# Kernel optimization log

Measured on AMD Instinct MI355X. Metric: run time of the kernel, lower is better.

## Reference

```python
import jax, jax.numpy as jnp
import numpy as np
import math

B, N, E = 1024, 128, 1024
IN_DIM, H, EDGE_DIM, L, OUT_DIM = 16, 128, 4, 4, 1


def setup_inputs() -> dict:
    key = jax.random.key(0)
    ks = jax.random.split(key, 32)
    def g(k, shape, scale):
        return jax.random.normal(k, shape, dtype=jnp.float32) * scale
    D_in = IN_DIM + 3
    s_in = 1.0 / math.sqrt(D_in)
    s_h = 1.0 / math.sqrt(H)
    inp = {
        'atom_types': jax.random.normal(ks[0], (B, N, IN_DIM), dtype=jnp.float32),
        'coords_spherical': jax.random.uniform(ks[1], (B, N, 3), dtype=jnp.float32),
        'edge_index': jax.random.randint(ks[2], (B, 2, E), 0, N, dtype=jnp.int32),
        'edge_attr': jax.random.uniform(ks[3], (B, E, EDGE_DIM), dtype=jnp.float32),
        # ComplexEmbedding: magnitude / phase linear maps
        'emb_Wm': g(ks[4], (D_in, H), s_in), 'emb_bm': jnp.zeros((H,), jnp.float32),
        'emb_Wp': g(ks[5], (D_in, H), s_in), 'emb_bp': jnp.zeros((H,), jnp.float32),
        # per-layer attention params (stacked over L layers)
        'Wq': g(ks[6], (L, H, H), s_h), 'bq': jnp.zeros((L, H), jnp.float32),
        'Wk': g(ks[7], (L, H, H), s_h), 'bk': jnp.zeros((L, H), jnp.float32),
        'Wvm': g(ks[8], (L, H, H), s_h), 'bvm': jnp.zeros((L, H), jnp.float32),
        'Wvp': g(ks[9], (L, H, H), s_h), 'bvp': jnp.zeros((L, H), jnp.float32),
        # EdgeBiasProjection: edge_attr -> scalar bias, plus learned distance penalty
        'We': g(ks[10], (L, EDGE_DIM, 1), 0.5), 'be': jnp.zeros((L, 1), jnp.float32),
        'dist_scale': jnp.full((L,), -0.5, jnp.float32),
        # LayerNorm over magnitude
        'ln_g': jnp.ones((L, H), jnp.float32), 'ln_b': jnp.zeros((L, H), jnp.float32),
        # RealProjection: concat(real, imag) -> hidden
        'rp_W': g(ks[11], (2 * H, H), 1.0 / math.sqrt(2 * H)), 'rp_b': jnp.zeros((H,), jnp.float32),
        # out_head: Linear(2H, H) -> SiLU -> Linear(H, out_dim)
        'h1_W': g(ks[12], (2 * H, H), 1.0 / math.sqrt(2 * H)), 'h1_b': jnp.zeros((H,), jnp.float32),
        'h2_W': g(ks[13], (H, OUT_DIM), s_h), 'h2_b': jnp.zeros((OUT_DIM,), jnp.float32),
    }
    return inp


def reference(atom_types, coords_spherical, edge_index, edge_attr,
              emb_Wm, emb_bm, emb_Wp, emb_bp,
              Wq, bq, Wk, bk, Wvm, bvm, Wvp, bvp,
              We, be, dist_scale, ln_g, ln_b,
              rp_W, rp_b, h1_W, h1_b, h2_W, h2_b):
    n_layers = Wq.shape[0]
    hidden = Wq.shape[-1]
    scale = 1.0 / math.sqrt(hidden)  # CAMBIO 1: sqrt(D) scaling

    def mol_fwd(feats, sph, ei, ea):
        n = feats.shape[0]
        x = jnp.concatenate([feats, sph], axis=-1)          # [N, in_dim+3]
        mag = x @ emb_Wm + emb_bm                            # [N, H]
        ph = x @ emb_Wp + emb_bp                             # [N, H]
        for l in range(n_layers):
            q = mag @ Wq[l] + bq[l]
            k = mag @ Wk[l] + bk[l]
            vm = mag @ Wvm[l] + bvm[l]
            vp = ph @ Wvp[l] + bvp[l]
            scores = (q @ k.T) * scale                       # [N, N]
            # CAMBIO 3/7: edge_attr -> scalar bias + learned distance penalty
            bvals = (ea @ We[l] + be[l])[:, 0] + dist_scale[l] * ea[:, 0]  # [E]
            bias = jnp.zeros((n, n), scores.dtype).at[ei[0], ei[1]].add(bvals)
            attn = jax.nn.softmax(scores + bias, axis=-1)
            new_mag = attn @ vm + mag                        # residual
            new_ph = attn @ vp + ph                          # residual
            # CAMBIO 6: LayerNorm over magnitude only
            mu = new_mag.mean(-1, keepdims=True)
            var = ((new_mag - mu) ** 2).mean(-1, keepdims=True)
            mag = ln_g[l] * (new_mag - mu) * jax.lax.rsqrt(var + 1e-5) + ln_b[l]
            ph = new_ph
        # CAMBIO 4: RealProjection concat(real, imag)
        real = mag * jnp.cos(ph)
        imag = mag * jnp.sin(ph)
        atom_repr = jnp.concatenate([real, imag], axis=-1) @ rp_W + rp_b  # [N, H]
        # CAMBIO 2: mean + sum pooling
        return jnp.concatenate([atom_repr.mean(0), atom_repr.sum(0)], axis=-1)  # [2H]

    pooled = jax.vmap(mol_fwd)(atom_types, coords_spherical, edge_index, edge_attr)  # [B, 2H]
    h = jax.nn.silu(pooled @ h1_W + h1_b)
    return h @ h2_W + h2_b                                   # [B, out_dim]
```

## Files before the change

### kernel.cpp

```cpp
#include <hip/hip_runtime.h>
#include <math.h>


typedef __attribute__((ext_vector_type(8)))  short s16x8;
typedef __attribute__((ext_vector_type(16))) float f32x16;

#define STR  136
#define LOFS 17408
#define MFMA(a, b, c) __builtin_amdgcn_mfma_f32_32x32x16_bf16(a, b, c, 0, 0, 0)
#define ROWP(reg) (((reg) & 3) + (((reg) >> 2) << 3) + (h5 << 2))

__device__ __forceinline__ unsigned short bfhi(float x) {
  unsigned u = __float_as_uint(x);
  return (unsigned short)((u + 0x7FFFu + ((u >> 16) & 1u)) >> 16);
}
__device__ __forceinline__ float bf2f(unsigned short h) {
  return __uint_as_float(((unsigned)h) << 16);
}

__device__ __forceinline__ void stageB64(short* SH, const f32x16& acc, int row,
                                         int colbase, int h5, float scl) {
  #pragma unroll
  for (int q = 0; q < 4; ++q) {
    int col = colbase + 8 * q + 4 * h5;
    float v0 = acc[4*q+0] * scl, v1 = acc[4*q+1] * scl;
    float v2 = acc[4*q+2] * scl, v3 = acc[4*q+3] * scl;
    unsigned short h0 = bfhi(v0), h1 = bfhi(v1), h2 = bfhi(v2), h3 = bfhi(v3);
    *(short4*)(SH + row * STR + col) = make_short4((short)h0,(short)h1,(short)h2,(short)h3);
    *(short4*)(SH + LOFS + row * STR + col) =
        make_short4((short)bfhi(v0 - bf2f(h0)), (short)bfhi(v1 - bf2f(h1)),
                    (short)bfhi(v2 - bf2f(h2)), (short)bfhi(v3 - bf2f(h3)));
  }
}

__device__ __forceinline__ void gemmTW2(f32x16* acc, const short* W, const short* BH,
                                        int mtile, int kbN, int ttb, int l31, int h5,
                                        int lane) {
  #pragma unroll 1
  for (int kb = 0; kb < kbN; ++kb) {
    const short* wp = W + (((mtile * 8 + kb) * 64 + lane) * 8);
    s16x8 ah = *(const s16x8*)wp;
    s16x8 al = *(const s16x8*)(wp + 32768);
    int k0 = kb * 16 + 8 * h5;
    #pragma unroll
    for (int j = 0; j < 2; ++j) {
      int brow = 32 * (ttb + j) + l31;
      s16x8 bh = *(const s16x8*)(BH + brow * STR + k0);
      s16x8 bl = *(const s16x8*)(BH + LOFS + brow * STR + k0);
      acc[j] = MFMA(ah, bh, acc[j]);
      acc[j] = MFMA(ah, bl, acc[j]);
      acc[j] = MFMA(al, bh, acc[j]);
    }
  }
}

__device__ __forceinline__ void gemmNW2(f32x16* acc, const short* AH, const short* W,
                                        int mblk, int ttb, int l31, int h5, int lane) {
  int arow = mblk + l31;
  #pragma unroll 1
  for (int kb = 0; kb < 8; ++kb) {
    int k0 = kb * 16 + 8 * h5;
    s16x8 ah = *(const s16x8*)(AH + arow * STR + k0);
    s16x8 al = *(const s16x8*)(AH + LOFS + arow * STR + k0);
    #pragma unroll
    for (int j = 0; j < 2; ++j) {
      const short* wp = W + ((((ttb + j) * 8 + kb) * 64 + lane) * 8);
      s16x8 bh = *(const s16x8*)wp;
      s16x8 bl = *(const s16x8*)(wp + 32768);
      acc[j] = MFMA(ah, bh, acc[j]);
      acc[j] = MFMA(ah, bl, acc[j]);
      acc[j] = MFMA(al, bh, acc[j]);
    }
  }
}

__device__ __forceinline__ void gemmLL2(f32x16* acc, const short* AH, const short* BH,
                                        int mblk, int ttb, int l31, int h5) {
  int arow = mblk + l31;
  #pragma unroll 1
  for (int kb = 0; kb < 8; ++kb) {
    int k0 = kb * 16 + 8 * h5;
    s16x8 ah = *(const s16x8*)(AH + arow * STR + k0);
    s16x8 al = *(const s16x8*)(AH + LOFS + arow * STR + k0);
    #pragma unroll
    for (int j = 0; j < 2; ++j) {
      int brow = 32 * (ttb + j) + l31;
      s16x8 bh = *(const s16x8*)(BH + brow * STR + k0);
      s16x8 bl = *(const s16x8*)(BH + LOFS + brow * STR + k0);
      acc[j] = MFMA(ah, bh, acc[j]);
      acc[j] = MFMA(ah, bl, acc[j]);
      acc[j] = MFMA(al, bh, acc[j]);
    }
  }
}

__global__ __launch_bounds__(256)
void prep0_kernel(const float* __restrict__ Wq, const float* __restrict__ Wk,
                  const float* __restrict__ bq,
                  float* __restrict__ wprime, float* __restrict__ u) {
  __shared__ float WkS[128 * 129];
  __shared__ float WqS[32 * 129];
  int l = blockIdx.x >> 2, ablk = blockIdx.x & 3;
  int t = threadIdx.x;
  const float* wk = Wk + (size_t)l * 16384;
  const float* wq = Wq + (size_t)l * 16384 + ablk * 32 * 128;
  for (int idx = t; idx < 16384; idx += 256)
    WkS[(idx >> 7) * 129 + (idx & 127)] = wk[idx];
  for (int idx = t; idx < 4096; idx += 256)
    WqS[(idx >> 7) * 129 + (idx & 127)] = wq[idx];
  __syncthreads();
  int a = t >> 3, bs = t & 7;
  float acc[16];
  #pragma unroll
  for (int j = 0; j < 16; ++j) acc[j] = 0.f;
  for (int c = 0; c < 128; ++c) {
    float qa = WqS[a * 129 + c];
    #pragma unroll
    for (int j = 0; j < 16; ++j) acc[j] += qa * WkS[(8 * j + bs) * 129 + c];
  }
  float* dst = wprime + ((size_t)l * 128 + ablk * 32 + a) * 128;
  #pragma unroll
  for (int j = 0; j < 16; ++j) dst[8 * j + bs] = acc[j];
  if (ablk == 0 && t < 128) {
    float s = 0.f;
    const float* bql = bq + l * 128;
    for (int c = 0; c < 128; ++c) s += WkS[t * 129 + c] * bql[c];
    u[l * 128 + t] = 0.08838834764831845f * s;
  }
}

__global__ __launch_bounds__(512)
void prep_kernel(const float* __restrict__ wprime,
                 const float* __restrict__ Wvm, const float* __restrict__ Wvp,
                 const float* __restrict__ rp_W,
                 const float* __restrict__ emb_Wm, const float* __restrict__ emb_Wp,
                 short* __restrict__ ws) {
  int mid = blockIdx.x >> 2, hblk = blockIdx.x & 3;
  int kb = threadIdx.x >> 6, lane = threadIdx.x & 63;
  const float* src;
  int krows = 128;
  if (mid < 4)        src = wprime + (size_t)mid * 16384;
  else if (mid < 8)   src = Wvm + (size_t)(mid - 4) * 16384;
  else if (mid < 12)  src = Wvp + (size_t)(mid - 8) * 16384;
  else if (mid == 12) src = rp_W;
  else if (mid == 13) src = rp_W + 16384;
  else if (mid == 14) { src = emb_Wm; krows = 19; }
  else                { src = emb_Wp; krows = 19; }
  int h = hblk * 32 + (lane & 31);
  int kbase = kb * 16 + ((lane >> 5) << 3);
  s16x8 H, L;
  #pragma unroll
  for (int j = 0; j < 8; ++j) {
    int k = kbase + j;
    float v = (k < krows) ? src[(size_t)k * 128 + h] : 0.f;
    unsigned short hi = bfhi(v);
    H[j] = (short)hi;
    L[j] = (short)bfhi(v - bf2f(hi));
  }
  short* dst = ws + (size_t)mid * 65536 + ((hblk * 8 + kb) * 64 + lane) * 8;
  *(s16x8*)dst = H;
  *(s16x8*)(dst + 32768) = L;
}

__global__ __launch_bounds__(512, 2)
void cpt_kernel(const float* __restrict__ atom_types,
                const float* __restrict__ coords,
                const int*   __restrict__ edge_index,
                const float* __restrict__ edge_attr,
                const float* __restrict__ emb_bm, const float* __restrict__ emb_bp,
                const float* __restrict__ bvm, const float* __restrict__ bvp,
                const float* __restrict__ We,  const float* __restrict__ be,
                const float* __restrict__ dist_scale,
                const float* __restrict__ ln_g, const float* __restrict__ ln_b,
                const float* __restrict__ rp_b,
                const float* __restrict__ h1_W, const float* __restrict__ h1_b,
                const float* __restrict__ h2_W, const float* __restrict__ h2_b,
                const short* __restrict__ wpre, const float* __restrict__ uArr,
                float* __restrict__ out)
{
  __shared__ __align__(16) short R1s[34816];
  __shared__ __align__(16) short R2s[34816];
  __shared__ float SCa[512];
  __shared__ float SCb[512];

  const int t = threadIdx.x, b = blockIdx.x;
  const int w = t >> 6, lane = t & 63, l31 = lane & 31, h5 = lane >> 5;
  const int wm = w >> 1, ttb = (w & 1) << 1;
  const int mblk = wm << 5;
  const float scale = 0.08838834764831845f;

  if (t < 128) {
    const float* xr = atom_types + ((size_t)b * 128 + t) * 16;
    const float* cr = coords + ((size_t)b * 128 + t) * 3;
    float xv[19];
    float4 a0 = *(const float4*)xr,       a1 = *(const float4*)(xr + 4);
    float4 a2 = *(const float4*)(xr + 8), a3 = *(const float4*)(xr + 12);
    xv[0]=a0.x; xv[1]=a0.y; xv[2]=a0.z; xv[3]=a0.w;
    xv[4]=a1.x; xv[5]=a1.y; xv[6]=a1.z; xv[7]=a1.w;
    xv[8]=a2.x; xv[9]=a2.y; xv[10]=a2.z; xv[11]=a2.w;
    xv[12]=a3.x; xv[13]=a3.y; xv[14]=a3.z; xv[15]=a3.w;
    xv[16]=cr[0]; xv[17]=cr[1]; xv[18]=cr[2];
    #pragma unroll
    for (int k = 0; k < 32; ++k) {
      float v = (k < 19) ? xv[k] : 0.f;
      unsigned short hh = bfhi(v);
      R1s[t * STR + k] = (short)hh;
      R1s[LOFS + t * STR + k] = (short)bfhi(v - bf2f(hh));
    }
  }
  __syncthreads();

  f32x16 magT[2], phT[2];
  {
    #pragma unroll
    for (int reg = 0; reg < 16; ++reg) {
      float bm = emb_bm[32 * wm + ROWP(reg)];
      float bp = emb_bp[32 * wm + ROWP(reg)];
      #pragma unroll
      for (int j = 0; j < 2; ++j) { magT[j][reg] = bm; phT[j][reg] = bp; }
    }
    gemmTW2(magT, wpre + (size_t)14 * 65536, R1s, wm, 2, ttb, l31, h5, lane);
    gemmTW2(phT,  wpre + (size_t)15 * 65536, R1s, wm, 2, ttb, l31, h5, lane);
  }

  for (int l = 0; l < 4; ++l) {
    const short* wpP  = wpre + (size_t)l * 65536;
    const short* wvmP = wpre + (size_t)(4 + l) * 65536;
    const short* wvpP = wpre + (size_t)(8 + l) * 65536;
    float* Bf = (float*)R2s;

    __syncthreads();
    #pragma unroll
    for (int j = 0; j < 2; ++j)
      stageB64(R1s, magT[j], 32 * (ttb + j) + l31, mblk, h5, 1.f);
    {
      float4 z4 = make_float4(0.f, 0.f, 0.f, 0.f);
      #pragma unroll
      for (int k = 0; k < 8; ++k) *(float4*)(Bf + (t + 512 * k) * 4) = z4;
    }
    {
      float ur[16];
      #pragma unroll
      for (int reg = 0; reg < 16; ++reg) ur[reg] = uArr[l * 128 + 32 * wm + ROWP(reg)];
      #pragma unroll
      for (int j = 0; j < 2; ++j) {
        float p = 0.f;
        #pragma unroll
        for (int reg = 0; reg < 16; ++reg) p += magT[j][reg] * ur[reg];
        p += __shfl_xor(p, 32);
        if (h5 == 0) SCa[wm * 128 + 32 * (ttb + j) + l31] = p;
      }
    }
    __syncthreads();

    {
      float w0 = We[l*4], w1 = We[l*4+1], w2 = We[l*4+2], w3 = We[l*4+3];
      float bel = be[l], dsl = dist_scale[l];
      #pragma unroll
      for (int k = 0; k < 2; ++k) {
        int e = t + 512 * k;
        int e0 = edge_index[(size_t)b * 2048 + e];
        int e1 = edge_index[(size_t)b * 2048 + 1024 + e];
        float4 ea = *(const float4*)(edge_attr + ((size_t)b * 1024 + e) * 4);
        float bv = ea.x*w0 + ea.y*w1 + ea.z*w2 + ea.w*w3 + bel + dsl*ea.x;
        atomicAdd(&Bf[e1 * 128 + e0], bv);
      }
    }

    f32x16 accT[2];
    #pragma unroll
    for (int j = 0; j < 2; ++j)
      #pragma unroll
      for (int reg = 0; reg < 16; ++reg) accT[j][reg] = 0.f;
    gemmTW2(accT, wpP, R1s, wm, 8, ttb, l31, h5, lane);
    __syncthreads();

    f32x16 accS[2];
    {
      float vj[16];
      #pragma unroll
      for (int reg = 0; reg < 16; ++reg) {
        int jj = 32 * wm + ROWP(reg);
        vj[reg] = SCa[jj] + SCa[128 + jj] + SCa[256 + jj] + SCa[384 + jj];
      }
      #pragma unroll
      for (int j = 0; j < 2; ++j) {
        #pragma unroll
        for (int reg = 0; reg < 16; ++reg)
          accS[j][reg] = Bf[(32 * wm + ROWP(reg)) * 128 + 32 * (ttb + j) + l31] + vj[reg];
      }
    }
    __syncthreads();
    #pragma unroll
    for (int j = 0; j < 2; ++j)
      stageB64(R2s, accT[j], 32 * (ttb + j) + l31, mblk, h5, scale);
    __syncthreads();

    gemmLL2(accS, R1s, R2s, mblk, ttb, l31, h5);

    #pragma unroll
    for (int j = 0; j < 2; ++j) {
      float m = accS[j][0];
      #pragma unroll
      for (int reg = 1; reg < 16; ++reg) m = fmaxf(m, accS[j][reg]);
      m = fmaxf(m, __shfl_xor(m, 32));
      if (h5 == 0) SCa[wm * 128 + 32 * (ttb + j) + l31] = m;
    }
    __syncthreads();
    #pragma unroll
    for (int j = 0; j < 2; ++j) {
      int i = 32 * (ttb + j) + l31;
      float mg = fmaxf(fmaxf(SCa[i], SCa[128 + i]), fmaxf(SCa[256 + i], SCa[384 + i]));
      float s = 0.f;
      #pragma unroll
      for (int reg = 0; reg < 16; ++reg) {
        float e = __expf(accS[j][reg] - mg);
        accS[j][reg] = e; s += e;
      }
      s += __shfl_xor(s, 32);
      if (h5 == 0) SCb[wm * 128 + i] = s;
    }
    __syncthreads();
    #pragma unroll
    for (int j = 0; j < 2; ++j) {
      int i = 32 * (ttb + j) + l31;
      float sg = SCb[i] + SCb[128 + i] + SCb[256 + i] + SCb[384 + i];
      float inv = 1.f / sg;
      #pragma unroll
      for (int reg = 0; reg < 16; ++reg) accS[j][reg] *= inv;
    }
    #pragma unroll
    for (int j = 0; j < 2; ++j)
      stageB64(R2s, accS[j], 32 * (ttb + j) + l31, mblk, h5, 1.f);

    {
      f32x16 accVM[2];
      #pragma unroll
      for (int j = 0; j < 2; ++j) {
        float bv = bvm[l * 128 + 32 * (ttb + j) + l31];
        #pragma unroll
        for (int reg = 0; reg < 16; ++reg) accVM[j][reg] = bv;
      }
      gemmNW2(accVM, R1s, wvmP, mblk, ttb, l31, h5, lane);
      __syncthreads();
      #pragma unroll
      for (int j = 0; j < 2; ++j)
        stageB64(R1s, accVM[j], 32 * (ttb + j) + l31, mblk, h5, 1.f);
      __syncthreads();
    }

    f32x16 accM[2];
    #pragma unroll
    for (int j = 0; j < 2; ++j) accM[j] = magT[j];
    gemmLL2(accM, R1s, R2s, mblk, ttb, l31, h5);

    {
      #pragma unroll
      for (int j = 0; j < 2; ++j) {
        float s = 0.f, q = 0.f;
        #pragma unroll
        for (int reg = 0; reg < 16; ++reg) { float v = accM[j][reg]; s += v; q += v*v; }
        s += __shfl_xor(s, 32); q += __shfl_xor(q, 32);
        if (h5 == 0) {
          SCa[wm * 128 + 32 * (ttb + j) + l31] = s;
          SCb[wm * 128 + 32 * (ttb + j) + l31] = q;
        }
      }
      __syncthreads();
      #pragma unroll
      for (int reg = 0; reg < 16; ++reg) {
        float gv = ln_g[l * 128 + 32 * wm + ROWP(reg)];
        float bv = ln_b[l * 128 + 32 * wm + ROWP(reg)];
        #pragma unroll
        for (int j = 0; j < 2; ++j) {
          int i = 32 * (ttb + j) + l31;
          float s = SCa[i] + SCa[128 + i] + SCa[256 + i] + SCa[384 + i];
          float q = SCb[i] + SCb[128 + i] + SCb[256 + i] + SCb[384 + i];
          float mu = s * (1.f / 128.f);
          float var = q * (1.f / 128.f) - mu * mu;
          float inv = 1.f / sqrtf(var + 1e-5f);
          magT[j][reg] = gv * ((accM[j][reg] - mu) * inv) + bv;
        }
      }
    }
    #pragma unroll
    for (int j = 0; j < 2; ++j)
      stageB64(R1s, phT[j], 32 * (ttb + j) + l31, mblk, h5, 1.f);
    __syncthreads();

    {
      f32x16 accV[2];
      #pragma unroll
      for (int j = 0; j < 2; ++j) {
        float bv = bvp[l * 128 + 32 * (ttb + j) + l31];
        #pragma unroll
        for (int reg = 0; reg < 16; ++reg) accV[j][reg] = bv;
      }
      gemmNW2(accV, R1s, wvpP, mblk, ttb, l31, h5, lane);
      __syncthreads();
      #pragma unroll
      for (int j = 0; j < 2; ++j)
        stageB64(R1s, accV[j], 32 * (ttb + j) + l31, mblk, h5, 1.f);
      __syncthreads();
    }

    f32x16 accP[2];
    #pragma unroll
    for (int j = 0; j < 2; ++j) accP[j] = phT[j];
    gemmLL2(accP, R1s, R2s, mblk, ttb, l31, h5);
    #pragma unroll
    for (int j = 0; j < 2; ++j) phT[j] = accP[j];
  }

  f32x16 reT[2], imT[2];
  #pragma unroll
  for (int j = 0; j < 2; ++j)
    #pragma unroll
    for (int reg = 0; reg < 16; ++reg) {
      float s_, c_;
      __sincosf(phT[j][reg], &s_, &c_);
      reT[j][reg] = magT[j][reg] * c_;
      imT[j][reg] = magT[j][reg] * s_;
    }
  __syncthreads();
  #pragma unroll
  for (int j = 0; j < 2; ++j) {
    stageB64(R1s, reT[j], 32 * (ttb + j) + l31, mblk, h5, 1.f);
    stageB64(R2s, imT[j], 32 * (ttb + j) + l31, mblk, h5, 1.f);
  }
  __syncthreads();
  f32x16 accR[2];
  #pragma unroll
  for (int reg = 0; reg < 16; ++reg) {
    float bv = rp_b[32 * wm + ROWP(reg)];
    #pragma unroll
    for (int j = 0; j < 2; ++j) accR[j][reg] = bv;
  }
  gemmTW2(accR, wpre + (size_t)12 * 65536, R1s, wm, 8, ttb, l31, h5, lane);
  gemmTW2(accR, wpre + (size_t)13 * 65536, R2s, wm, 8, ttb, l31, h5, lane);

  {
    float cs[16];
    #pragma unroll
    for (int reg = 0; reg < 16; ++reg) {
      float s = accR[0][reg] + accR[1][reg];
      s += __shfl_xor(s, 16); s += __shfl_xor(s, 8);
      s += __shfl_xor(s, 4);  s += __shfl_xor(s, 2); s += __shfl_xor(s, 1);
      cs[reg] = s;
    }
    if (l31 == 0) {
      #pragma unroll
      for (int reg = 0; reg < 16; ++reg)
        SCa[(w & 1) * 128 + 32 * wm + ROWP(reg)] = cs[reg];
    }
  }
  __syncthreads();
  if (t < 128) {
    float acc = h1_b[t];
    for (int i = 0; i < 128; ++i) {
      float c = SCa[i] + SCa[128 + i];
      acc += c * (h1_W[(size_t)i * 128 + t] * (1.f / 128.f) +
                  h1_W[(size_t)(128 + i) * 128 + t]);
    }
    float hv = acc / (1.f + __expf(-acc));
    SCb[t] = hv * h2_W[t];
  }
  __syncthreads();
  if (t < 64) {
    float s2 = SCb[t] + SCb[64 + t];
    #pragma unroll
    for (int off = 32; off >= 1; off >>= 1) s2 += __shfl_xor(s2, off);
    if (t == 0) out[b] = s2 + h2_b[0];
  }
}

extern "C" void kernel_launch(void* const* d_in, const int* in_sizes, int n_in,
                              void* d_out, int out_size, void* d_ws, size_t ws_size,
                              hipStream_t stream) {
  const float* atom_types = (const float*)d_in[0];
  const float* coords     = (const float*)d_in[1];
  const int*   edge_index = (const int*)  d_in[2];
  const float* edge_attr  = (const float*)d_in[3];
  const float* emb_Wm = (const float*)d_in[4];
  const float* emb_bm = (const float*)d_in[5];
  const float* emb_Wp = (const float*)d_in[6];
  const float* emb_bp = (const float*)d_in[7];
  const float* Wq  = (const float*)d_in[8];
  const float* bq  = (const float*)d_in[9];
  const float* Wk  = (const float*)d_in[10];
  const float* bk  = (const float*)d_in[11];
  const float* Wvm = (const float*)d_in[12];
  const float* bvm = (const float*)d_in[13];
  const float* Wvp = (const float*)d_in[14];
  const float* bvp = (const float*)d_in[15];
  const float* We  = (const float*)d_in[16];
  const float* be  = (const float*)d_in[17];
  const float* dist_scale = (const float*)d_in[18];
  const float* ln_g = (const float*)d_in[19];
  const float* ln_b = (const float*)d_in[20];
  const float* rp_W = (const float*)d_in[21];
  const float* rp_b = (const float*)d_in[22];
  const float* h1_W = (const float*)d_in[23];
  const float* h1_b = (const float*)d_in[24];
  const float* h2_W = (const float*)d_in[25];
  const float* h2_b = (const float*)d_in[26];
  float* out = (float*)d_out;
  (void)bk;
  short* wpre   = (short*)d_ws;
  float* uArr   = (float*)((char*)d_ws + (size_t)16 * 131072);
  float* wprime = (float*)((char*)d_ws + (size_t)16 * 131072 + 2048);

  hipLaunchKernelGGL(prep0_kernel, dim3(16), dim3(256), 0, stream,
                     Wq, Wk, bq, wprime, uArr);
  hipLaunchKernelGGL(prep_kernel, dim3(64), dim3(512), 0, stream,
                     wprime, Wvm, Wvp, rp_W, emb_Wm, emb_Wp, wpre);
  hipLaunchKernelGGL(cpt_kernel, dim3(1024), dim3(512), 0, stream,
                     atom_types, coords, edge_index, edge_attr,
                     emb_bm, emb_bp,
                     bvm, bvp,
                     We, be, dist_scale, ln_g, ln_b,
                     rp_b, h1_W, h1_b, h2_W, h2_b,
                     (const short*)wpre, (const float*)uArr, out);
}
```

Measured before the change: 621.8 us.

## Double block to 1024 threads with one 32x32 output tile per wave

The per-molecule kernel now launches 1024 threads (16 waves) instead of 512. Each wave owns a single 32-column tile rather than two, and all GEMM helpers, softmax, LayerNorm and the final reductions are rewritten for one accumulator per wave. Since shared memory limits each CU to about one block, the aim is twice as many resident waves to hide LDS and global latency, and fewer registers per thread. The cost is that each wave reloads its A/weight fragments on its own, so the per-MFMA load traffic is roughly doubled, and 1024-thread barriers get more expensive.

Measured after the change: 758.3 us. 22.0% more time.

```diff
diff --git a/kernel.cpp b/kernel.cpp
--- a/kernel.cpp
+++ b/kernel.cpp
@@ -33,64 +33,55 @@
   }
 }
 
-__device__ __forceinline__ void gemmTW2(f32x16* acc, const short* W, const short* BH,
-                                        int mtile, int kbN, int ttb, int l31, int h5,
+__device__ __forceinline__ void gemmTW1(f32x16& acc, const short* W, const short* BH,
+                                        int mtile, int kbN, int tt, int l31, int h5,
                                         int lane) {
+  int brow = 32 * tt + l31;
   #pragma unroll 1
   for (int kb = 0; kb < kbN; ++kb) {
     const short* wp = W + (((mtile * 8 + kb) * 64 + lane) * 8);
     s16x8 ah = *(const s16x8*)wp;
     s16x8 al = *(const s16x8*)(wp + 32768);
     int k0 = kb * 16 + 8 * h5;
-    #pragma unroll
-    for (int j = 0; j < 2; ++j) {
-      int brow = 32 * (ttb + j) + l31;
-      s16x8 bh = *(const s16x8*)(BH + brow * STR + k0);
-      s16x8 bl = *(const s16x8*)(BH + LOFS + brow * STR + k0);
-      acc[j] = MFMA(ah, bh, acc[j]);
-      acc[j] = MFMA(ah, bl, acc[j]);
-      acc[j] = MFMA(al, bh, acc[j]);
-    }
-  }
-}
-
-__device__ __forceinline__ void gemmNW2(f32x16* acc, const short* AH, const short* W,
-                                        int mblk, int ttb, int l31, int h5, int lane) {
+    s16x8 bh = *(const s16x8*)(BH + brow * STR + k0);
+    s16x8 bl = *(const s16x8*)(BH + LOFS + brow * STR + k0);
+    acc = MFMA(ah, bh, acc);
+    acc = MFMA(ah, bl, acc);
+    acc = MFMA(al, bh, acc);
+  }
+}
+
+__device__ __forceinline__ void gemmNW1(f32x16& acc, const short* AH, const short* W,
+                                        int mblk, int tt, int l31, int h5, int lane) {
   int arow = mblk + l31;
   #pragma unroll 1
   for (int kb = 0; kb < 8; ++kb) {
     int k0 = kb * 16 + 8 * h5;
     s16x8 ah = *(const s16x8*)(AH + arow * STR + k0);
     s16x8 al = *(const s16x8*)(AH + LOFS + arow * STR + k0);
-    #pragma unroll
-    for (int j = 0; j < 2; ++j) {
-      const short* wp = W + ((((ttb + j) * 8 + kb) * 64 + lane) * 8);
-      s16x8 bh = *(const s16x8*)wp;
-      s16x8 bl = *(const s16x8*)(wp + 32768);
-      acc[j] = MFMA(ah, bh, acc[j]);
-      acc[j] = MFMA(ah, bl, acc[j]);
-      acc[j] = MFMA(al, bh, acc[j]);
-    }
-  }
-}
-
-__device__ __forceinline__ void gemmLL2(f32x16* acc, const short* AH, const short* BH,
-                                        int mblk, int ttb, int l31, int h5) {
+    const short* wp = W + (((tt * 8 + kb) * 64 + lane) * 8);
+    s16x8 bh = *(const s16x8*)wp;
+    s16x8 bl = *(const s16x8*)(wp + 32768);
+    acc = MFMA(ah, bh, acc);
+    acc = MFMA(ah, bl, acc);
+    acc = MFMA(al, bh, acc);
+  }
+}
+
+__device__ __forceinline__ void gemmLL1(f32x16& acc, const short* AH, const short* BH,
+                                        int mblk, int tt, int l31, int h5) {
   int arow = mblk + l31;
+  int brow = 32 * tt + l31;
   #pragma unroll 1
   for (int kb = 0; kb < 8; ++kb) {
     int k0 = kb * 16 + 8 * h5;
     s16x8 ah = *(const s16x8*)(AH + arow * STR + k0);
     s16x8 al = *(const s16x8*)(AH + LOFS + arow * STR + k0);
-    #pragma unroll
-    for (int j = 0; j < 2; ++j) {
-      int brow = 32 * (ttb + j) + l31;
-      s16x8 bh = *(const s16x8*)(BH + brow * STR + k0);
-      s16x8 bl = *(const s16x8*)(BH + LOFS + brow * STR + k0);
-      acc[j] = MFMA(ah, bh, acc[j]);
-      acc[j] = MFMA(ah, bl, acc[j]);
-      acc[j] = MFMA(al, bh, acc[j]);
-    }
+    s16x8 bh = *(const s16x8*)(BH + brow * STR + k0);
+    s16x8 bl = *(const s16x8*)(BH + LOFS + brow * STR + k0);
+    acc = MFMA(ah, bh, acc);
+    acc = MFMA(ah, bl, acc);
+    acc = MFMA(al, bh, acc);
   }
 }
 
@@ -162,7 +153,7 @@
   *(s16x8*)(dst + 32768) = L;
 }
 
-__global__ __launch_bounds__(512, 2)
+__global__ __launch_bounds__(1024, 4)
 void cpt_kernel(const float* __restrict__ atom_types,
                 const float* __restrict__ coords,
                 const int*   __restrict__ edge_index,
@@ -185,8 +176,9 @@
 
   const int t = threadIdx.x, b = blockIdx.x;
   const int w = t >> 6, lane = t & 63, l31 = lane & 31, h5 = lane >> 5;
-  const int wm = w >> 1, ttb = (w & 1) << 1;
+  const int wm = w >> 2, tt = w & 3;
   const int mblk = wm << 5;
+  const int myrow = 32 * tt + l31;
   const float scale = 0.08838834764831845f;
 
   if (t < 128) {
@@ -210,17 +202,15 @@
   }
   __syncthreads();
 
-  f32x16 magT[2], phT[2];
+  f32x16 magT, phT;
   {
     #pragma unroll
     for (int reg = 0; reg < 16; ++reg) {
-      float bm = emb_bm[32 * wm + ROWP(reg)];
-      float bp = emb_bp[32 * wm + ROWP(reg)];
-      #pragma unroll
-      for (int j = 0; j < 2; ++j) { magT[j][reg] = bm; phT[j][reg] = bp; }
-    }
-    gemmTW2(magT, wpre + (size_t)14 * 65536, R1s, wm, 2, ttb, l31, h5, lane);
-    gemmTW2(phT,  wpre + (size_t)15 * 65536, R1s, wm, 2, ttb, l31, h5, lane);
+      magT[reg] = emb_bm[32 * wm + ROWP(reg)];
+      phT[reg]  = emb_bp[32 * wm + ROWP(reg)];
+    }
+    gemmTW1(magT, wpre + (size_t)14 * 65536, R1s, wm, 2, tt, l31, h5, lane);
+    gemmTW1(phT,  wpre + (size_t)15 * 65536, R1s, wm, 2, tt, l31, h5, lane);
   }
 
   for (int l = 0; l < 4; ++l) {
@@ -230,220 +220,157 @@
     float* Bf = (float*)R2s;
 
     __syncthreads();
-    #pragma unroll
-    for (int j = 0; j < 2; ++j)
-      stageB64(R1s, magT[j], 32 * (ttb + j) + l31, mblk, h5, 1.f);
+    stageB64(R1s, magT, myrow, mblk, h5, 1.f);
     {
       float4 z4 = make_float4(0.f, 0.f, 0.f, 0.f);
       #pragma unroll
-      for (int k = 0; k < 8; ++k) *(float4*)(Bf + (t + 512 * k) * 4) = z4;
-    }
-    {
-      float ur[16];
-      #pragma unroll
-      for (int reg = 0; reg < 16; ++reg) ur[reg] = uArr[l * 128 + 32 * wm + ROWP(reg)];
-      #pragma unroll
-      for (int j = 0; j < 2; ++j) {
-        float p = 0.f;
-        #pragma unroll
-        for (int reg = 0; reg < 16; ++reg) p += magT[j][reg] * ur[reg];
-        p += __shfl_xor(p, 32);
-        if (h5 == 0) SCa[wm * 128 + 32 * (ttb + j) + l31] = p;
-      }
+      for (int k = 0; k < 4; ++k) *(float4*)(Bf + (t + 1024 * k) * 4) = z4;
+    }
+    {
+      float p = 0.f;
+      #pragma unroll
+      for (int reg = 0; reg < 16; ++reg)
+        p += magT[reg] * uArr[l * 128 + 32 * wm + ROWP(reg)];
+      p += __shfl_xor(p, 32);
+      if (h5 == 0) SCa[wm * 128 + myrow] = p;
     }
     __syncthreads();
 
     {
       float w0 = We[l*4], w1 = We[l*4+1], w2 = We[l*4+2], w3 = We[l*4+3];
       float bel = be[l], dsl = dist_scale[l];
-      #pragma unroll
-      for (int k = 0; k < 2; ++k) {
-        int e = t + 512 * k;
-        int e0 = edge_index[(size_t)b * 2048 + e];
-        int e1 = edge_index[(size_t)b * 2048 + 1024 + e];
-        float4 ea = *(const float4*)(edge_attr + ((size_t)b * 1024 + e) * 4);
-        float bv = ea.x*w0 + ea.y*w1 + ea.z*w2 + ea.w*w3 + bel + dsl*ea.x;
-        atomicAdd(&Bf[e1 * 128 + e0], bv);
-      }
-    }
-
-    f32x16 accT[2];
-    #pragma unroll
-    for (int j = 0; j < 2; ++j)
-      #pragma unroll
-      for (int reg = 0; reg < 16; ++reg) accT[j][reg] = 0.f;
-    gemmTW2(accT, wpP, R1s, wm, 8, ttb, l31, h5, lane);
-    __syncthreads();
-
-    f32x16 accS[2];
-    {
-      float vj[16];
-      #pragma unroll
-      for (int reg = 0; reg < 16; ++reg) {
-        int jj = 32 * wm + ROWP(reg);
-        vj[reg] = SCa[jj] + SCa[128 + jj] + SCa[256 + jj] + SCa[384 + jj];
-      }
-      #pragma unroll
-      for (int j = 0; j < 2; ++j) {
-        #pragma unroll
-        for (int reg = 0; reg < 16; ++reg)
-          accS[j][reg] = Bf[(32 * wm + ROWP(reg)) * 128 + 32 * (ttb + j) + l31] + vj[reg];
-      }
-    }
-    __syncthreads();
-    #pragma unroll
-    for (int j = 0; j < 2; ++j)
-      stageB64(R2s, accT[j], 32 * (ttb + j) + l31, mblk, h5, scale);
-    __syncthreads();
-
-    gemmLL2(accS, R1s, R2s, mblk, ttb, l31, h5);
-
-    #pragma unroll
-    for (int j = 0; j < 2; ++j) {
-      float m = accS[j][0];
-      #pragma unroll
-      for (int reg = 1; reg < 16; ++reg) m = fmaxf(m, accS[j][reg]);
+      int e0 = edge_index[(size_t)b * 2048 + t];
+      int e1 = edge_index[(size_t)b * 2048 + 1024 + t];
+      float4 ea = *(const float4*)(edge_attr + ((size_t)b * 1024 + t) * 4);
+      float bv = ea.x*w0 + ea.y*w1 + ea.z*w2 + ea.w*w3 + bel + dsl*ea.x;
+      atomicAdd(&Bf[e1 * 128 + e0], bv);
+    }
+
+    f32x16 accT;
+    #pragma unroll
+    for (int reg = 0; reg < 16; ++reg) accT[reg] = 0.f;
+    gemmTW1(accT, wpP, R1s, wm, 8, tt, l31, h5, lane);
+    __syncthreads();
+
+    f32x16 accS;
+    #pragma unroll
+    for (int reg = 0; reg < 16; ++reg) {
+      int jj = 32 * wm + ROWP(reg);
+      float vj = SCa[jj] + SCa[128 + jj] + SCa[256 + jj] + SCa[384 + jj];
+      accS[reg] = Bf[jj * 128 + myrow] + vj;
+    }
+    __syncthreads();
+    stageB64(R2s, accT, myrow, mblk, h5, scale);
+    __syncthreads();
+
+    gemmLL1(accS, R1s, R2s, mblk, tt, l31, h5);
+
+    {
+      float m = accS[0];
+      #pragma unroll
+      for (int reg = 1; reg < 16; ++reg) m = fmaxf(m, accS[reg]);
       m = fmaxf(m, __shfl_xor(m, 32));
-      if (h5 == 0) SCa[wm * 128 + 32 * (ttb + j) + l31] = m;
-    }
-    __syncthreads();
-    #pragma unroll
-    for (int j = 0; j < 2; ++j) {
-      int i = 32 * (ttb + j) + l31;
+      if (h5 == 0) SCa[wm * 128 + myrow] = m;
+    }
+    __syncthreads();
+    {
+      int i = myrow;
       float mg = fmaxf(fmaxf(SCa[i], SCa[128 + i]), fmaxf(SCa[256 + i], SCa[384 + i]));
       float s = 0.f;
       #pragma unroll
       for (int reg = 0; reg < 16; ++reg) {
-        float e = __expf(accS[j][reg] - mg);
-        accS[j][reg] = e; s += e;
+        float e = __expf(accS[reg] - mg);
+        accS[reg] = e; s += e;
       }
       s += __shfl_xor(s, 32);
       if (h5 == 0) SCb[wm * 128 + i] = s;
     }
     __syncthreads();
-    #pragma unroll
-    for (int j = 0; j < 2; ++j) {
-      int i = 32 * (ttb + j) + l31;
+    {
+      int i = myrow;
       float sg = SCb[i] + SCb[128 + i] + SCb[256 + i] + SCb[384 + i];
       float inv = 1.f / sg;
       #pragma unroll
-      for (int reg = 0; reg < 16; ++reg) accS[j][reg] *= inv;
-    }
-    #pragma unroll
-    for (int j = 0; j < 2; ++j)
-      stageB64(R2s, accS[j], 32 * (ttb + j) + l31, mblk, h5, 1.f);
-
-    {
-      f32x16 accVM[2];
-      #pragma unroll
-      for (int j = 0; j < 2; ++j) {
-        float bv = bvm[l * 128 + 32 * (ttb + j) + l31];
-        #pragma unroll
-        for (int reg = 0; reg < 16; ++reg) accVM[j][reg] = bv;
-      }
-      gemmNW2(accVM, R1s, wvmP, mblk, ttb, l31, h5, lane);
+      for (int reg = 0; reg < 16; ++reg) accS[reg] *= inv;
+    }
+    stageB64(R2s, accS, myrow, mblk, h5, 1.f);
+
+    {
+      f32x16 accVM;
+      float bv = bvm[l * 128 + myrow];
+      #pragma unroll
+      for (int reg = 0; reg < 16; ++reg) accVM[reg] = bv;
+      gemmNW1(accVM, R1s, wvmP, mblk, tt, l31, h5, lane);
       __syncthreads();
-      #pragma unroll
-      for (int j = 0; j < 2; ++j)
-        stageB64(R1s, accVM[j], 32 * (ttb + j) + l31, mblk, h5, 1.f);
+      stageB64(R1s, accVM, myrow, mblk, h5, 1.f);
       __syncthreads();
     }
 
-    f32x16 accM[2];
-    #pragma unroll
-    for (int j = 0; j < 2; ++j) accM[j] = magT[j];
-    gemmLL2(accM, R1s, R2s, mblk, ttb, l31, h5);
-
-    {
-      #pragma unroll
-      for (int j = 0; j < 2; ++j) {
-        float s = 0.f, q = 0.f;
-        #pragma unroll
-        for (int reg = 0; reg < 16; ++reg) { float v = accM[j][reg]; s += v; q += v*v; }
-        s += __shfl_xor(s, 32); q += __shfl_xor(q, 32);
-        if (h5 == 0) {
-          SCa[wm * 128 + 32 * (ttb + j) + l31] = s;
-          SCb[wm * 128 + 32 * (ttb + j) + l31] = q;
-        }
-      }
+    f32x16 accM = magT;
+    gemmLL1(accM, R1s, R2s, mblk, tt, l31, h5);
+
+    {
+      float s = 0.f, q = 0.f;
+      #pragma unroll
+      for (int reg = 0; reg < 16; ++reg) { float v = accM[reg]; s += v; q += v*v; }
+      s += __shfl_xor(s, 32); q += __shfl_xor(q, 32);
+      if (h5 == 0) { SCa[wm * 128 + myrow] = s; SCb[wm * 128 + myrow] = q; }
       __syncthreads();
+      int i = myrow;
+      float ss = SCa[i] + SCa[128 + i] + SCa[256 + i] + SCa[384 + i];
+      float qq = SCb[i] + SCb[128 + i] + SCb[256 + i] + SCb[384 + i];
+      float mu = ss * (1.f / 128.f);
+      float var = qq * (1.f / 128.f) - mu * mu;
+      float inv = 1.f / sqrtf(var + 1e-5f);
       #pragma unroll
       for (int reg = 0; reg < 16; ++reg) {
         float gv = ln_g[l * 128 + 32 * wm + ROWP(reg)];
         float bv = ln_b[l * 128 + 32 * wm + ROWP(reg)];
-        #pragma unroll
-        for (int j = 0; j < 2; ++j) {
-          int i = 32 * (ttb + j) + l31;
-          float s = SCa[i] + SCa[128 + i] + SCa[256 + i] + SCa[384 + i];
-          float q = SCb[i] + SCb[128 + i] + SCb[256 + i] + SCb[384 + i];
-          float mu = s * (1.f / 128.f);
-          float var = q * (1.f / 128.f) - mu * mu;
-          float inv = 1.f / sqrtf(var + 1e-5f);
-          magT[j][reg] = gv * ((accM[j][reg] - mu) * inv) + bv;
-        }
+        magT[reg] = gv * ((accM[reg] - mu) * inv) + bv;
       }
     }
-    #pragma unroll
-    for (int j = 0; j < 2; ++j)
-      stageB64(R1s, phT[j], 32 * (ttb + j) + l31, mblk, h5, 1.f);
-    __syncthreads();
-
-    {
-      f32x16 accV[2];
-      #pragma unroll
-      for (int j = 0; j < 2; ++j) {
-        float bv = bvp[l * 128 + 32 * (ttb + j) + l31];
-        #pragma unroll
-        for (int reg = 0; reg < 16; ++reg) accV[j][reg] = bv;
-      }
-      gemmNW2(accV, R1s, wvpP, mblk, ttb, l31, h5, lane);
+    stageB64(R1s, phT, myrow, mblk, h5, 1.f);
+    __syncthreads();
+
+    {
+      f32x16 accV;
+      float bv = bvp[l * 128 + myrow];
+      #pragma unroll
+      for (int reg = 0; reg < 16; ++reg) accV[reg] = bv;
+      gemmNW1(accV, R1s, wvpP, mblk, tt, l31, h5, lane);
       __syncthreads();
-      #pragma unroll
-      for (int j = 0; j < 2; ++j)
-        stageB64(R1s, accV[j], 32 * (ttb + j) + l31, mblk, h5, 1.f);
+      stageB64(R1s, accV, myrow, mblk, h5, 1.f);
       __syncthreads();
     }
 
-    f32x16 accP[2];
-    #pragma unroll
-    for (int j = 0; j < 2; ++j) accP[j] = phT[j];
-    gemmLL2(accP, R1s, R2s, mblk, ttb, l31, h5);
-    #pragma unroll
-    for (int j = 0; j < 2; ++j) phT[j] = accP[j];
-  }
-
-  f32x16 reT[2], imT[2];
-  #pragma unroll
-  for (int j = 0; j < 2; ++j)
-    #pragma unroll
-    for (int reg = 0; reg < 16; ++reg) {
-      float s_, c_;
-      __sincosf(phT[j][reg], &s_, &c_);
-      reT[j][reg] = magT[j][reg] * c_;
-      imT[j][reg] = magT[j][reg] * s_;
-    }
-  __syncthreads();
-  #pragma unroll
-  for (int j = 0; j < 2; ++j) {
-    stageB64(R1s, reT[j], 32 * (ttb + j) + l31, mblk, h5, 1.f);
-    stageB64(R2s, imT[j], 32 * (ttb + j) + l31, mblk, h5, 1.f);
-  }
-  __syncthreads();
-  f32x16 accR[2];
+    f32x16 accP = phT;
+    gemmLL1(accP, R1s, R2s, mblk, tt, l31, h5);
+    phT = accP;
+  }
+
+  f32x16 reT, imT;
   #pragma unroll
   for (int reg = 0; reg < 16; ++reg) {
-    float bv = rp_b[32 * wm + ROWP(reg)];
-    #pragma unroll
-    for (int j = 0; j < 2; ++j) accR[j][reg] = bv;
-  }
-  gemmTW2(accR, wpre + (size_t)12 * 65536, R1s, wm, 8, ttb, l31, h5, lane);
-  gemmTW2(accR, wpre + (size_t)13 * 65536, R2s, wm, 8, ttb, l31, h5, lane);
+    float s_, c_;
+    __sincosf(phT[reg], &s_, &c_);
+    reT[reg] = magT[reg] * c_;
+    imT[reg] = magT[reg] * s_;
+  }
+  __syncthreads();
+  stageB64(R1s, reT, myrow, mblk, h5, 1.f);
+  stageB64(R2s, imT, myrow, mblk, h5, 1.f);
+  __syncthreads();
+  f32x16 accR;
+  #pragma unroll
+  for (int reg = 0; reg < 16; ++reg) accR[reg] = rp_b[32 * wm + ROWP(reg)];
+  gemmTW1(accR, wpre + (size_t)12 * 65536, R1s, wm, 8, tt, l31, h5, lane);
+  gemmTW1(accR, wpre + (size_t)13 * 65536, R2s, wm, 8, tt, l31, h5, lane);
 
   {
     float cs[16];
     #pragma unroll
     for (int reg = 0; reg < 16; ++reg) {
-      float s = accR[0][reg] + accR[1][reg];
+      float s = accR[reg];
       s += __shfl_xor(s, 16); s += __shfl_xor(s, 8);
       s += __shfl_xor(s, 4);  s += __shfl_xor(s, 2); s += __shfl_xor(s, 1);
       cs[reg] = s;
@@ -451,14 +378,14 @@
     if (l31 == 0) {
       #pragma unroll
       for (int reg = 0; reg < 16; ++reg)
-        SCa[(w & 1) * 128 + 32 * wm + ROWP(reg)] = cs[reg];
+        SCa[tt * 128 + 32 * wm + ROWP(reg)] = cs[reg];
     }
   }
   __syncthreads();
   if (t < 128) {
     float acc = h1_b[t];
     for (int i = 0; i < 128; ++i) {
-      float c = SCa[i] + SCa[128 + i];
+      float c = SCa[i] + SCa[128 + i] + SCa[256 + i] + SCa[384 + i];
       acc += c * (h1_W[(size_t)i * 128 + t] * (1.f / 128.f) +
                   h1_W[(size_t)(128 + i) * 128 + t]);
     }
@@ -514,7 +441,7 @@
                      Wq, Wk, bq, wprime, uArr);
   hipLaunchKernelGGL(prep_kernel, dim3(64), dim3(512), 0, stream,
                      wprime, Wvm, Wvp, rp_W, emb_Wm, emb_Wp, wpre);
-  hipLaunchKernelGGL(cpt_kernel, dim3(1024), dim3(512), 0, stream,
+  hipLaunchKernelGGL(cpt_kernel, dim3(1024), dim3(1024), 0, stream,
                      atom_types, coords, edge_index, edge_attr,
                      emb_bm, emb_bp,
                      bvm, bvp,
```
